# Optimization experiments

Hardware: AMD Instinct MI355X
Metric: run time of the kernel (lower is better)

## Reference

```python
import jax, jax.numpy as jnp
import numpy as np

B, S, DA, DV, DU, L, M = 16, 256, 1, 32, 1, 4, 12


def conv1x1(x, w, b):
    # x: [B,C,H,W], w: [O,C], b: [O]
    return jnp.einsum('bchw,oc->bohw', x, w) + b[None, :, None, None]


def setup_inputs() -> dict:
    key = jax.random.key(0)
    ks = jax.random.split(key, 12)
    sc = 0.02
    return {
        'x':    jax.random.normal(ks[0], (B, S, S, DA), dtype=jnp.float32),
        'p_w':  sc * jax.random.normal(ks[1], (DV, DA + 2), dtype=jnp.float32),
        'p_b':  sc * jax.random.normal(ks[2], (DV,), dtype=jnp.float32),
        'ws_w': sc * jax.random.normal(ks[3], (L, DV, DV), dtype=jnp.float32),
        'ws_b': sc * jax.random.normal(ks[4], (L, DV), dtype=jnp.float32),
        'w1r':  sc * jax.random.normal(ks[5], (L, DV, DV, M, M), dtype=jnp.float32),
        'w1i':  sc * jax.random.normal(ks[6], (L, DV, DV, M, M), dtype=jnp.float32),
        'w2r':  sc * jax.random.normal(ks[7], (L, DV, DV, M, M), dtype=jnp.float32),
        'w2i':  sc * jax.random.normal(ks[8], (L, DV, DV, M, M), dtype=jnp.float32),
        'q_w':  sc * jax.random.normal(ks[9], (DU, DV), dtype=jnp.float32),
        'q_b':  sc * jax.random.normal(ks[10], (DU,), dtype=jnp.float32),
    }


def fourier_layer(x, w1r, w1i, w2r, w2i):
    # x: [B,C,H,W]; FFT norm None == 'backward' (numpy/jax default)
    b, c, h, w = x.shape
    x_ft = jnp.fft.rfft2(x)                       # [B,C,H,W//2+1] complex
    W1 = w1r + 1j * w1i                           # [C,C,M,M]
    W2 = w2r + 1j * w2i
    top = jnp.einsum('bixy,ioxy->boxy', x_ft[:, :, :M, :M], W1)
    bot = jnp.einsum('bixy,ioxy->boxy', x_ft[:, :, -M:, :M], W2)
    out_ft = jnp.zeros((b, c, h, w // 2 + 1), dtype=x_ft.dtype)
    out_ft = out_ft.at[:, :, :M, :M].set(top)
    out_ft = out_ft.at[:, :, h - M:, :M].set(bot)
    return jnp.fft.irfft2(out_ft, s=(h, w))


def reference(x, p_w, p_b, ws_w, ws_b, w1r, w1i, w2r, w2i, q_w, q_b):
    b, sx, sy, _ = x.shape
    # grid as in get_grid (requires sx == sy, as the original implicitly does)
    gx = jnp.linspace(-1.0, 1.0, sx, dtype=jnp.float32)
    gy = jnp.linspace(-1.0, 1.0, sy, dtype=jnp.float32)
    gridx = jnp.broadcast_to(gx.reshape(1, 1, sx, 1), (b, sy, sx, 1))
    gridy = jnp.broadcast_to(gy.reshape(1, sy, 1, 1), (b, sy, sx, 1))
    grid = jnp.concatenate([gridy, gridx], axis=-1)     # [B,Sy,Sx,2]
    h = jnp.concatenate([x, grid], axis=-1)             # [B,S,S,DA+2]
    h = jnp.transpose(h, (0, 3, 1, 2))                  # NCHW
    h = conv1x1(h, p_w, p_b)                            # lifting
    for i in range(L):
        x1 = fourier_layer(h, w1r[i], w1i[i], w2r[i], w2i[i])
        x2 = conv1x1(h, ws_w[i], ws_b[i])
        h = x1 + x2
        if i < L - 1:
            h = jax.nn.relu(h)
    h = conv1x1(h, q_w, q_b)                            # projection -> [B,1,S,S]
    return jnp.transpose(h, (0, 2, 3, 1)).squeeze(-1)   # [B,S,S]
```

## Files before the change

kernel.cpp:

```cpp
#include <hip/hip_runtime.h>
#include <math.h>

#define NB 16
#define SS 256
#define DV 32
#define MM 12
#define MK 24
#define LL 4
#define TWO_PI_N 0.024543692606170259679f
#define TSTR 65


__global__ __launch_bounds__(256) void k_prep(const float* __restrict__ ws_w,
        float* __restrict__ twT, float* __restrict__ wT, float* __restrict__ tw2)
{
    int j = threadIdx.x;
    #pragma unroll
    for (int k = 0; k < MM; ++k) {
        float ang = TWO_PI_N * (float)((k * j) & 255);
        float s, c; sincosf(ang, &s, &c);
        twT[j * (MM * 2) + 2 * k]     = c;
        twT[j * (MM * 2) + 2 * k + 1] = -s;
        tw2[(k * SS + j) * 2]     = c;
        tw2[(k * SS + j) * 2 + 1] = s;
    }
    for (int idx = threadIdx.x; idx < LL * DV * DV; idx += 256) {
        int l = idx >> 10, rem = idx & 1023, co = rem >> 5, ci = rem & 31;
        wT[(l * DV + ci) * DV + co] = ws_w[(l * DV + co) * DV + ci];
    }
}

__global__ __launch_bounds__(256) void k_lift(const float* __restrict__ x,
        const float* __restrict__ p_w, const float* __restrict__ p_b,
        float* __restrict__ h)
{
    int tid = threadIdx.x;
    int lane = tid & 63;
    int w = __builtin_amdgcn_readfirstlane(tid >> 6);
    int b  = blockIdx.x >> 6;
    int iy = ((blockIdx.x & 63) << 2) + w;
    int j0 = lane << 2;

    float4 xv = *(const float4*)(x + ((size_t)(b * SS + iy)) * SS + j0);
    float gy = -1.f + 2.f * (float)iy * (1.f / 255.f);
    float4 gx;
    gx.x = -1.f + 2.f * (float)j0 * (1.f / 255.f);
    gx.y = gx.x + 2.f / 255.f; gx.z = gx.y + 2.f / 255.f; gx.w = gx.z + 2.f / 255.f;

    float* hb = h + ((size_t)b * DV * SS + iy) * SS + j0;
    #pragma unroll
    for (int c = 0; c < DV; ++c) {
        float w0 = p_w[3*c], w1 = p_w[3*c+1], w2 = p_w[3*c+2], bb = p_b[c];
        float4 v;
        v.x = w0 * xv.x + w1 * gy + w2 * gx.x + bb;
        v.y = w0 * xv.y + w1 * gy + w2 * gx.y + bb;
        v.z = w0 * xv.z + w1 * gy + w2 * gx.z + bb;
        v.w = w0 * xv.w + w1 * gy + w2 * gx.w + bb;
        *(float4*)(hb + (size_t)c * SS * SS) = v;
    }
}

__global__ __launch_bounds__(512, 4) void k_rowdft(const float* __restrict__ h,
        const float* __restrict__ twT, float* __restrict__ A)
{
    __shared__ float smem[SS * TSTR];
    int tid = threadIdx.x;
    int iy = tid & 255;
    int half = __builtin_amdgcn_readfirstlane(tid >> 8);
    int b = blockIdx.x >> 5, c = blockIdx.x & 31;
    const float* hrow = h + (size_t)blockIdx.x * SS * SS;

    float ar[MM], ai[MM];
    #pragma unroll
    for (int k = 0; k < MM; ++k) { ar[k] = 0.f; ai[k] = 0.f; }

    for (int t = 0; t < 4; ++t) {
        int jb = t * 64;
        __syncthreads();
        #pragma unroll
        for (int k = 0; k < 8; ++k) {
            int idx = tid + k * 512;
            int row = idx >> 4, col4 = idx & 15;
            float4 v = *(const float4*)(hrow + (size_t)row * SS + jb + col4 * 4);
            float* d = &smem[row * TSTR + col4 * 4];
            d[0] = v.x; d[1] = v.y; d[2] = v.z; d[3] = v.w;
        }
        __syncthreads();
        const float* rp = &smem[iy * TSTR + half * 32];
        #pragma unroll
        for (int jq = 0; jq < 8; ++jq) {
            #pragma unroll
            for (int u = 0; u < 4; ++u) {
                float v = rp[jq * 4 + u];
                const float* twj = twT + (size_t)(jb + half * 32 + jq * 4 + u)
                                         * (MM * 2);
                #pragma unroll
                for (int k = 0; k < 6; ++k) {
                    ar[2*k]   += v * twj[4*k];
                    ai[2*k]   += v * twj[4*k + 1];
                    ar[2*k+1] += v * twj[4*k + 2];
                    ai[2*k+1] += v * twj[4*k + 3];
                }
            }
        }
    }

    __syncthreads();
    if (half == 0) {
        #pragma unroll
        for (int k = 0; k < MM; ++k) {
            smem[(2*k) * SS + iy]     = ar[k];
            smem[(2*k + 1) * SS + iy] = ai[k];
        }
    }
    __syncthreads();
    if (half == 1) {
        #pragma unroll
        for (int ky = 0; ky < MM; ++ky) {
            float2 val;
            val.x = ar[ky] + smem[(2*ky) * SS + iy];
            val.y = ai[ky] + smem[(2*ky + 1) * SS + iy];
            size_t o = ((((size_t)b * MM + ky) * DV + c) * SS + iy) * 2;
            *(float2*)&A[o] = val;
        }
    }
}

__global__ __launch_bounds__(256, 4) void k_cm(const float* __restrict__ A,
        const float* __restrict__ w1r, const float* __restrict__ w1i,
        const float* __restrict__ w2r, const float* __restrict__ w2i,
        float* __restrict__ F, int l)
{
    __shared__ float FinS[DV][6][2];
    int blk = blockIdx.x;
    int mg = blk & 3;
    int bk = blk >> 2;
    int ky = bk % MM;
    int tid = threadIdx.x;
    int c = tid >> 3, ch = tid & 7;
    int iy0 = ch * 32;

    const float2* Ap = (const float2*)(A + ((size_t)bk * DV + c) * SS * 2);

    float fr[6], fi[6], pc[6], ps[6], sc[6], ssn[6];
    #pragma unroll
    for (int k = 0; k < 6; ++k) {
        int m = mg * 6 + k;
        int f = (m < MM) ? m : (232 + m);
        float s, cc;
        sincosf(TWO_PI_N * (float)f, &s, &cc);
        sc[k] = cc; ssn[k] = s;
        sincosf(TWO_PI_N * (float)((f * iy0) & 255), &s, &cc);
        pc[k] = cc; ps[k] = s;
        fr[k] = fi[k] = 0.f;
    }
    #pragma unroll 4
    for (int i = 0; i < 32; ++i) {
        float2 a = Ap[iy0 + i];
        #pragma unroll
        for (int k = 0; k < 6; ++k) {
            fr[k] += a.x * pc[k] + a.y * ps[k];
            fi[k] += a.y * pc[k] - a.x * ps[k];
            float np = pc[k] * sc[k] - ps[k] * ssn[k];
            float nq = pc[k] * ssn[k] + ps[k] * sc[k];
            pc[k] = np; ps[k] = nq;
        }
    }
    #pragma unroll
    for (int m = 1; m < 8; m <<= 1) {
        #pragma unroll
        for (int k = 0; k < 6; ++k) {
            fr[k] += __shfl_xor(fr[k], m, 64);
            fi[k] += __shfl_xor(fi[k], m, 64);
        }
    }
    #pragma unroll
    for (int k = 0; k < 6; ++k) {
        if (ch == k) { FinS[c][k][0] = fr[k]; FinS[c][k][1] = fi[k]; }
    }
    __syncthreads();

    if (ch < 6) {
        int o = c;
        int m = mg * 6 + ch;
        const float* Wr; const float* Wi; int xm;
        if (m < MM) { Wr = w1r; Wi = w1i; xm = m; }
        else        { Wr = w2r; Wi = w2i; xm = m - MM; }
        float scale = ((ky == 0) ? 1.0f : 2.0f) * (1.0f / 65536.0f);
        float orr = 0.f, oii = 0.f;
        #pragma unroll 4
        for (int i = 0; i < DV; ++i) {
            float gr = FinS[i][ch][0], gi = FinS[i][ch][1];
            size_t wi = ((size_t)(l * DV + i) * DV + o) * (MM * MM) + xm * MM + ky;
            float wr = Wr[wi], wim = Wi[wi];
            orr += gr * wr - gi * wim;
            oii += gr * wim + gi * wr;
        }
        size_t off = (((size_t)bk * MK + m) * DV + o) * 2;
        F[off] = orr * scale; F[off + 1] = oii * scale;
    }
}

__global__ __launch_bounds__(384) void k_inv1(const float* __restrict__ F,
        float* __restrict__ g)
{
    __shared__ float itw[MK * 2];
    int tid = threadIdx.x;
    int b = blockIdx.x >> 8, iy = blockIdx.x & 255;
    if (tid < MK) {
        int f = (tid < MM) ? tid : (232 + tid);
        float ang = TWO_PI_N * (float)((f * iy) & 255);
        float s, c; sincosf(ang, &s, &c);
        itw[2 * tid] = c; itw[2 * tid + 1] = s;
    }
    __syncthreads();

    int ky = tid >> 5, co = tid & 31;
    const float* Fp = F + ((size_t)(b * MM + ky) * MK) * (DV * 2) + 2 * co;
    float gr = 0.f, gi = 0.f;
    #pragma unroll
    for (int m = 0; m < MK; ++m) {
        float2 fv = *(const float2*)(Fp + (size_t)m * (DV * 2));
        float ic = itw[2 * m], is = itw[2 * m + 1];
        gr += fv.x * ic - fv.y * is;
        gi += fv.x * is + fv.y * ic;
    }
    size_t o = (((size_t)(b * SS + iy)) * MM + ky) * (DV * 2) + 2 * co;
    g[o] = gr; g[o + 1] = gi;
}

template<int FINAL>
__global__ __launch_bounds__(256, 4) void k_pt(float* __restrict__ h,
        const float* __restrict__ g, const float* __restrict__ wT,
        const float* __restrict__ ws_b, const float* __restrict__ tw2,
        const float* __restrict__ q_w, const float* __restrict__ q_b,
        float* __restrict__ out, int l)
{
    int tid = threadIdx.x;
    int lane = tid & 63;
    int w = __builtin_amdgcn_readfirstlane(tid >> 6);
    int b  = blockIdx.x >> 7;
    int iy = ((blockIdx.x & 127) << 1) + (w >> 1);
    int j0 = ((w & 1) << 7) + (lane << 1);

    float* hb = h + ((size_t)b * DV * SS + iy) * SS + j0;
    const float* wt  = wT + (size_t)l * DV * DV;
    const float* wsb = ws_b + (size_t)l * DV;

    float2 acc[DV];
    #pragma unroll
    for (int co = 0; co < DV; ++co) {
        float bv = wsb[co];
        acc[co].x = bv; acc[co].y = bv;
    }

    #pragma unroll 4
    for (int ci = 0; ci < DV; ++ci) {
        float2 hv = *(const float2*)(hb + (size_t)ci * SS * SS);
        const float* wc = wt + ci * DV;
        #pragma unroll
        for (int co = 0; co < DV; ++co) {
            float wv = wc[co];
            acc[co].x += wv * hv.x; acc[co].y += wv * hv.y;
        }
    }

    const float* gp = g + ((size_t)(b * SS + iy)) * (MM * DV * 2);
    #pragma unroll 2
    for (int ky = 0; ky < MM; ++ky) {
        float4 t4 = *(const float4*)(tw2 + ((size_t)ky * SS + j0) * 2);
        const float* Gk = gp + ky * (DV * 2);
        #pragma unroll
        for (int co = 0; co < DV; ++co) {
            float gr = Gk[2 * co], gi = Gk[2 * co + 1];
            acc[co].x += gr * t4.x - gi * t4.y;
            acc[co].y += gr * t4.z - gi * t4.w;
        }
    }

    if (FINAL) {
        float qb = q_b[0];
        float2 o2; o2.x = qb; o2.y = qb;
        #pragma unroll
        for (int co = 0; co < DV; ++co) {
            float qv = q_w[co];
            o2.x += qv * acc[co].x; o2.y += qv * acc[co].y;
        }
        *(float2*)(out + ((size_t)(b * SS + iy)) * SS + j0) = o2;
    } else {
        #pragma unroll
        for (int co = 0; co < DV; ++co) {
            float2 v;
            v.x = fmaxf(acc[co].x, 0.f); v.y = fmaxf(acc[co].y, 0.f);
            *(float2*)(hb + (size_t)co * SS * SS) = v;
        }
    }
}

extern "C" void kernel_launch(void* const* d_in, const int* in_sizes, int n_in,
                              void* d_out, int out_size, void* d_ws, size_t ws_size,
                              hipStream_t stream)
{
    const float* x    = (const float*)d_in[0];
    const float* p_w  = (const float*)d_in[1];
    const float* p_b  = (const float*)d_in[2];
    const float* ws_w = (const float*)d_in[3];
    const float* ws_b = (const float*)d_in[4];
    const float* w1r  = (const float*)d_in[5];
    const float* w1i  = (const float*)d_in[6];
    const float* w2r  = (const float*)d_in[7];
    const float* w2i  = (const float*)d_in[8];
    const float* q_w  = (const float*)d_in[9];
    const float* q_b  = (const float*)d_in[10];
    float* out = (float*)d_out;

    float* h   = (float*)d_ws;
    float* A   = h   + (size_t)NB * DV * SS * SS;
    float* F   = A   + (size_t)NB * MM * DV * SS * 2;
    float* g   = F   + (size_t)NB * MM * MK * DV * 2;
    float* twT = g   + (size_t)NB * SS * MM * DV * 2;
    float* wT  = twT + (size_t)SS * MM * 2;
    float* tw2 = wT  + (size_t)LL * DV * DV;

    dim3 blk(256);
    k_prep<<<1, blk, 0, stream>>>(ws_w, twT, wT, tw2);
    k_lift<<<NB * 64, blk, 0, stream>>>(x, p_w, p_b, h);
    for (int l = 0; l < LL; ++l) {
        k_rowdft<<<NB * DV, dim3(512), 0, stream>>>(h, twT, A);
        k_cm<<<NB * MM * 4, blk, 0, stream>>>(A, w1r, w1i, w2r, w2i, F, l);
        k_inv1<<<NB * SS, dim3(384), 0, stream>>>(F, g);
        if (l < LL - 1)
            k_pt<0><<<NB * 128, blk, 0, stream>>>(h, g, wT, ws_b, tw2,
                                                  nullptr, nullptr, nullptr, l);
        else
            k_pt<1><<<NB * 128, blk, 0, stream>>>(h, g, wT, ws_b, tw2,
                                                  q_w, q_b, out, l);
    }
}
```

Baseline: 708.3 us.

## Fuse row DFT into lift and pointwise kernels via LDS staging

Removes the standalone row-DFT kernel. The lift and pointwise-update kernels now also stage their freshly computed h rows (2 rows × 32 channels) in LDS and compute the truncated row DFT from there, writing A directly. This avoids re-reading the full h tensor from global memory for each layer and drops one launch per layer. In exchange the fused kernels need more LDS and run at lower occupancy (launch bounds 2). The per-thread DFT loop also covers 64 samples serially, followed by an LDS reduction across 4 wave partials.

```diff
diff --git a/kernel.cpp b/kernel.cpp
--- a/kernel.cpp
+++ b/kernel.cpp
@@ -8,7 +8,7 @@
 #define MK 24
 #define LL 4
 #define TWO_PI_N 0.024543692606170259679f
-#define TSTR 65
+#define TSTR2 258
 
 
 __global__ __launch_bounds__(256) void k_prep(const float* __restrict__ ws_w,
@@ -30,100 +30,87 @@
     }
 }
 
-__global__ __launch_bounds__(256) void k_lift(const float* __restrict__ x,
+__device__ __forceinline__ void row_dft_lds(float* smem,
+        const float* __restrict__ twT, float* __restrict__ A,
+        int b, int iyp, int tid)
+{
+    int lane = tid & 63;
+    int jq = __builtin_amdgcn_readfirstlane(tid >> 6);
+    int row = lane >> 5, c = lane & 31;
+
+    const float* rp = &smem[(row * DV + c) * TSTR2 + jq * 64];
+    float ar[MM], ai[MM];
+    #pragma unroll
+    for (int k = 0; k < MM; ++k) { ar[k] = 0.f; ai[k] = 0.f; }
+
+    #pragma unroll 4
+    for (int i = 0; i < 64; ++i) {
+        float v = rp[i];
+        const float* twj = twT + (size_t)(jq * 64 + i) * (MM * 2);
+        #pragma unroll
+        for (int k = 0; k < 6; ++k) {
+            ar[2*k]   += v * twj[4*k];
+            ai[2*k]   += v * twj[4*k + 1];
+            ar[2*k+1] += v * twj[4*k + 2];
+            ai[2*k+1] += v * twj[4*k + 3];
+        }
+    }
+
+    __syncthreads();
+    float* pp = &smem[(size_t)((jq * 2 + row) * DV + c) * 25];
+    #pragma unroll
+    for (int k = 0; k < MM; ++k) { pp[2*k] = ar[k]; pp[2*k + 1] = ai[k]; }
+    __syncthreads();
+
+    int row2 = tid >> 7, c2 = (tid >> 2) & 31, kg = tid & 3;
+    int iy = iyp * 2 + row2;
+    #pragma unroll
+    for (int kk = 0; kk < 3; ++kk) {
+        int ky = kg * 3 + kk;
+        float sr = 0.f, si = 0.f;
+        #pragma unroll
+        for (int q = 0; q < 4; ++q) {
+            const float* qq = &smem[(size_t)((q * 2 + row2) * DV + c2) * 25 + 2 * ky];
+            sr += qq[0]; si += qq[1];
+        }
+        size_t o = ((((size_t)b * MM + ky) * DV + c2) * SS + iy) * 2;
+        float2 val; val.x = sr; val.y = si;
+        *(float2*)&A[o] = val;
+    }
+}
+
+__global__ __launch_bounds__(256, 2) void k_liftA(const float* __restrict__ x,
         const float* __restrict__ p_w, const float* __restrict__ p_b,
-        float* __restrict__ h)
-{
+        float* __restrict__ h, const float* __restrict__ twT,
+        float* __restrict__ A)
+{
+    __shared__ float smem[2 * DV * TSTR2];
     int tid = threadIdx.x;
     int lane = tid & 63;
     int w = __builtin_amdgcn_readfirstlane(tid >> 6);
-    int b  = blockIdx.x >> 6;
-    int iy = ((blockIdx.x & 63) << 2) + w;
-    int j0 = lane << 2;
-
-    float4 xv = *(const float4*)(x + ((size_t)(b * SS + iy)) * SS + j0);
-    float gy = -1.f + 2.f * (float)iy * (1.f / 255.f);
-    float4 gx;
-    gx.x = -1.f + 2.f * (float)j0 * (1.f / 255.f);
-    gx.y = gx.x + 2.f / 255.f; gx.z = gx.y + 2.f / 255.f; gx.w = gx.z + 2.f / 255.f;
+    int b   = blockIdx.x >> 7;
+    int iyp = blockIdx.x & 127;
+    int row = w >> 1;
+    int iy  = iyp * 2 + row;
+    int j0  = ((w & 1) << 7) + (lane << 1);
+
+    float2 xv = *(const float2*)(x + ((size_t)(b * SS + iy)) * SS + j0);
+    float gy  = -1.f + 2.f * (float)iy * (1.f / 255.f);
+    float gxa = -1.f + 2.f * (float)j0 * (1.f / 255.f);
+    float gxb = gxa + 2.f / 255.f;
 
     float* hb = h + ((size_t)b * DV * SS + iy) * SS + j0;
     #pragma unroll
     for (int c = 0; c < DV; ++c) {
         float w0 = p_w[3*c], w1 = p_w[3*c+1], w2 = p_w[3*c+2], bb = p_b[c];
-        float4 v;
-        v.x = w0 * xv.x + w1 * gy + w2 * gx.x + bb;
-        v.y = w0 * xv.y + w1 * gy + w2 * gx.y + bb;
-        v.z = w0 * xv.z + w1 * gy + w2 * gx.z + bb;
-        v.w = w0 * xv.w + w1 * gy + w2 * gx.w + bb;
-        *(float4*)(hb + (size_t)c * SS * SS) = v;
-    }
-}
-
-__global__ __launch_bounds__(512, 4) void k_rowdft(const float* __restrict__ h,
-        const float* __restrict__ twT, float* __restrict__ A)
-{
-    __shared__ float smem[SS * TSTR];
-    int tid = threadIdx.x;
-    int iy = tid & 255;
-    int half = __builtin_amdgcn_readfirstlane(tid >> 8);
-    int b = blockIdx.x >> 5, c = blockIdx.x & 31;
-    const float* hrow = h + (size_t)blockIdx.x * SS * SS;
-
-    float ar[MM], ai[MM];
-    #pragma unroll
-    for (int k = 0; k < MM; ++k) { ar[k] = 0.f; ai[k] = 0.f; }
-
-    for (int t = 0; t < 4; ++t) {
-        int jb = t * 64;
-        __syncthreads();
-        #pragma unroll
-        for (int k = 0; k < 8; ++k) {
-            int idx = tid + k * 512;
-            int row = idx >> 4, col4 = idx & 15;
-            float4 v = *(const float4*)(hrow + (size_t)row * SS + jb + col4 * 4);
-            float* d = &smem[row * TSTR + col4 * 4];
-            d[0] = v.x; d[1] = v.y; d[2] = v.z; d[3] = v.w;
-        }
-        __syncthreads();
-        const float* rp = &smem[iy * TSTR + half * 32];
-        #pragma unroll
-        for (int jq = 0; jq < 8; ++jq) {
-            #pragma unroll
-            for (int u = 0; u < 4; ++u) {
-                float v = rp[jq * 4 + u];
-                const float* twj = twT + (size_t)(jb + half * 32 + jq * 4 + u)
-                                         * (MM * 2);
-                #pragma unroll
-                for (int k = 0; k < 6; ++k) {
-                    ar[2*k]   += v * twj[4*k];
-                    ai[2*k]   += v * twj[4*k + 1];
-                    ar[2*k+1] += v * twj[4*k + 2];
-                    ai[2*k+1] += v * twj[4*k + 3];
-                }
-            }
-        }
-    }
-
-    __syncthreads();
-    if (half == 0) {
-        #pragma unroll
-        for (int k = 0; k < MM; ++k) {
-            smem[(2*k) * SS + iy]     = ar[k];
-            smem[(2*k + 1) * SS + iy] = ai[k];
-        }
-    }
-    __syncthreads();
-    if (half == 1) {
-        #pragma unroll
-        for (int ky = 0; ky < MM; ++ky) {
-            float2 val;
-            val.x = ar[ky] + smem[(2*ky) * SS + iy];
-            val.y = ai[ky] + smem[(2*ky + 1) * SS + iy];
-            size_t o = ((((size_t)b * MM + ky) * DV + c) * SS + iy) * 2;
-            *(float2*)&A[o] = val;
-        }
-    }
+        float2 v;
+        v.x = w0 * xv.x + w1 * gy + w2 * gxa + bb;
+        v.y = w0 * xv.y + w1 * gy + w2 * gxb + bb;
+        *(float2*)(hb + (size_t)c * SS * SS) = v;
+        *(float2*)&smem[(size_t)(row * DV + c) * TSTR2 + j0] = v;
+    }
+    __syncthreads();
+    row_dft_lds(smem, twT, A, b, iyp, tid);
 }
 
 __global__ __launch_bounds__(256, 4) void k_cm(const float* __restrict__ A,
@@ -229,8 +216,68 @@
     g[o] = gr; g[o + 1] = gi;
 }
 
-template<int FINAL>
-__global__ __launch_bounds__(256, 4) void k_pt(float* __restrict__ h,
+__global__ __launch_bounds__(256, 2) void k_ptA(float* __restrict__ h,
+        const float* __restrict__ g, const float* __restrict__ wT,
+        const float* __restrict__ ws_b, const float* __restrict__ tw2,
+        const float* __restrict__ twT, float* __restrict__ A, int l)
+{
+    __shared__ float smem[2 * DV * TSTR2];
+    int tid = threadIdx.x;
+    int lane = tid & 63;
+    int w = __builtin_amdgcn_readfirstlane(tid >> 6);
+    int b   = blockIdx.x >> 7;
+    int iyp = blockIdx.x & 127;
+    int row = w >> 1;
+    int iy  = iyp * 2 + row;
+    int j0  = ((w & 1) << 7) + (lane << 1);
+
+    float* hb = h + ((size_t)b * DV * SS + iy) * SS + j0;
+    const float* wt  = wT + (size_t)l * DV * DV;
+    const float* wsb = ws_b + (size_t)l * DV;
+
+    float2 acc[DV];
+    #pragma unroll
+    for (int co = 0; co < DV; ++co) {
+        float bv = wsb[co];
+        acc[co].x = bv; acc[co].y = bv;
+    }
+
+    #pragma unroll 4
+    for (int ci = 0; ci < DV; ++ci) {
+        float2 hv = *(const float2*)(hb + (size_t)ci * SS * SS);
+        const float* wc = wt + ci * DV;
+        #pragma unroll
+        for (int co = 0; co < DV; ++co) {
+            float wv = wc[co];
+            acc[co].x += wv * hv.x; acc[co].y += wv * hv.y;
+        }
+    }
+
+    const float* gp = g + ((size_t)(b * SS + iy)) * (MM * DV * 2);
+    #pragma unroll 2
+    for (int ky = 0; ky < MM; ++ky) {
+        float4 t4 = *(const float4*)(tw2 + ((size_t)ky * SS + j0) * 2);
+        const float* Gk = gp + ky * (DV * 2);
+        #pragma unroll
+        for (int co = 0; co < DV; ++co) {
+            float gr = Gk[2 * co], gi = Gk[2 * co + 1];
+            acc[co].x += gr * t4.x - gi * t4.y;
+            acc[co].y += gr * t4.z - gi * t4.w;
+        }
+    }
+
+    #pragma unroll
+    for (int co = 0; co < DV; ++co) {
+        float2 v;
+        v.x = fmaxf(acc[co].x, 0.f); v.y = fmaxf(acc[co].y, 0.f);
+        *(float2*)(hb + (size_t)co * SS * SS) = v;
+        *(float2*)&smem[(size_t)(row * DV + co) * TSTR2 + j0] = v;
+    }
+    __syncthreads();
+    row_dft_lds(smem, twT, A, b, iyp, tid);
+}
+
+__global__ __launch_bounds__(256, 4) void k_final(const float* __restrict__ h,
         const float* __restrict__ g, const float* __restrict__ wT,
         const float* __restrict__ ws_b, const float* __restrict__ tw2,
         const float* __restrict__ q_w, const float* __restrict__ q_b,
@@ -243,7 +290,7 @@
     int iy = ((blockIdx.x & 127) << 1) + (w >> 1);
     int j0 = ((w & 1) << 7) + (lane << 1);
 
-    float* hb = h + ((size_t)b * DV * SS + iy) * SS + j0;
+    const float* hb = h + ((size_t)b * DV * SS + iy) * SS + j0;
     const float* wt  = wT + (size_t)l * DV * DV;
     const float* wsb = ws_b + (size_t)l * DV;
 
@@ -278,23 +325,14 @@
         }
     }
 
-    if (FINAL) {
-        float qb = q_b[0];
-        float2 o2; o2.x = qb; o2.y = qb;
-        #pragma unroll
-        for (int co = 0; co < DV; ++co) {
-            float qv = q_w[co];
-            o2.x += qv * acc[co].x; o2.y += qv * acc[co].y;
-        }
-        *(float2*)(out + ((size_t)(b * SS + iy)) * SS + j0) = o2;
-    } else {
-        #pragma unroll
-        for (int co = 0; co < DV; ++co) {
-            float2 v;
-            v.x = fmaxf(acc[co].x, 0.f); v.y = fmaxf(acc[co].y, 0.f);
-            *(float2*)(hb + (size_t)co * SS * SS) = v;
-        }
-    }
+    float qb = q_b[0];
+    float2 o2; o2.x = qb; o2.y = qb;
+    #pragma unroll
+    for (int co = 0; co < DV; ++co) {
+        float qv = q_w[co];
+        o2.x += qv * acc[co].x; o2.y += qv * acc[co].y;
+    }
+    *(float2*)(out + ((size_t)(b * SS + iy)) * SS + j0) = o2;
 }
 
 extern "C" void kernel_launch(void* const* d_in, const int* in_sizes, int n_in,
@@ -324,16 +362,14 @@
 
     dim3 blk(256);
     k_prep<<<1, blk, 0, stream>>>(ws_w, twT, wT, tw2);
-    k_lift<<<NB * 64, blk, 0, stream>>>(x, p_w, p_b, h);
+    k_liftA<<<NB * 128, blk, 0, stream>>>(x, p_w, p_b, h, twT, A);
     for (int l = 0; l < LL; ++l) {
-        k_rowdft<<<NB * DV, dim3(512), 0, stream>>>(h, twT, A);
         k_cm<<<NB * MM * 4, blk, 0, stream>>>(A, w1r, w1i, w2r, w2i, F, l);
         k_inv1<<<NB * SS, dim3(384), 0, stream>>>(F, g);
         if (l < LL - 1)
-            k_pt<0><<<NB * 128, blk, 0, stream>>>(h, g, wT, ws_b, tw2,
-                                                  nullptr, nullptr, nullptr, l);
+            k_ptA<<<NB * 128, blk, 0, stream>>>(h, g, wT, ws_b, tw2, twT, A, l);
         else
-            k_pt<1><<<NB * 128, blk, 0, stream>>>(h, g, wT, ws_b, tw2,
+            k_final<<<NB * 128, blk, 0, stream>>>(h, g, wT, ws_b, tw2,
                                                   q_w, q_b, out, l);
     }
 }
```

Result: slower. 787.0 us (+11.1%).

## Split row DFT across two half-row blocks with 4-way column partition

Applied to the files above, without the earlier changes.

The row-DFT kernel now launches two blocks per (batch, channel) plane, each handling 128 rows. The 512 threads split the columns four ways in 32-column tiles, using a smaller shared buffer, and combine partial sums with a two-step shared-memory tree reduction. This doubles the grid and shrinks LDS use so more blocks fit per CU, at the cost of extra reduction syncs. Launch-bound occupancy hints are also raised for k_rowdft and k_pt.

```diff
diff --git a/kernel.cpp b/kernel.cpp
--- a/kernel.cpp
+++ b/kernel.cpp
@@ -8,7 +8,7 @@
 #define MK 24
 #define LL 4
 #define TWO_PI_N 0.024543692606170259679f
-#define TSTR 65
+#define TSTR 33
 
 
 __global__ __launch_bounds__(256) void k_prep(const float* __restrict__ ws_w,
@@ -60,67 +60,84 @@
     }
 }
 
-__global__ __launch_bounds__(512, 4) void k_rowdft(const float* __restrict__ h,
+__global__ __launch_bounds__(512, 8) void k_rowdft(const float* __restrict__ h,
         const float* __restrict__ twT, float* __restrict__ A)
 {
-    __shared__ float smem[SS * TSTR];
-    int tid = threadIdx.x;
-    int iy = tid & 255;
-    int half = __builtin_amdgcn_readfirstlane(tid >> 8);
-    int b = blockIdx.x >> 5, c = blockIdx.x & 31;
-    const float* hrow = h + (size_t)blockIdx.x * SS * SS;
+    __shared__ float smem[6336];
+    int tid = threadIdx.x;
+    int iy = tid & 127;
+    int jq = __builtin_amdgcn_readfirstlane(tid >> 7);
+    int bc = blockIdx.x >> 1;
+    int iyh = blockIdx.x & 1;
+    int b = bc >> 5, c = bc & 31;
+    const float* hrow = h + (size_t)bc * SS * SS + (size_t)iyh * 128 * SS;
 
     float ar[MM], ai[MM];
     #pragma unroll
     for (int k = 0; k < MM; ++k) { ar[k] = 0.f; ai[k] = 0.f; }
 
-    for (int t = 0; t < 4; ++t) {
-        int jb = t * 64;
+    for (int t = 0; t < 8; ++t) {
+        int jb = t * 32;
         __syncthreads();
         #pragma unroll
-        for (int k = 0; k < 8; ++k) {
+        for (int k = 0; k < 2; ++k) {
             int idx = tid + k * 512;
-            int row = idx >> 4, col4 = idx & 15;
+            int row = idx >> 3, col4 = idx & 7;
             float4 v = *(const float4*)(hrow + (size_t)row * SS + jb + col4 * 4);
             float* d = &smem[row * TSTR + col4 * 4];
             d[0] = v.x; d[1] = v.y; d[2] = v.z; d[3] = v.w;
         }
         __syncthreads();
-        const float* rp = &smem[iy * TSTR + half * 32];
-        #pragma unroll
-        for (int jq = 0; jq < 8; ++jq) {
+        const float* rp = &smem[iy * TSTR + jq * 8];
+        #pragma unroll
+        for (int i = 0; i < 8; ++i) {
+            float v = rp[i];
+            const float* twj = twT + (size_t)(jb + jq * 8 + i) * (MM * 2);
             #pragma unroll
-            for (int u = 0; u < 4; ++u) {
-                float v = rp[jq * 4 + u];
-                const float* twj = twT + (size_t)(jb + half * 32 + jq * 4 + u)
-                                         * (MM * 2);
-                #pragma unroll
-                for (int k = 0; k < 6; ++k) {
-                    ar[2*k]   += v * twj[4*k];
-                    ai[2*k]   += v * twj[4*k + 1];
-                    ar[2*k+1] += v * twj[4*k + 2];
-                    ai[2*k+1] += v * twj[4*k + 3];
-                }
+            for (int k = 0; k < 6; ++k) {
+                ar[2*k]   += v * twj[4*k];
+                ai[2*k]   += v * twj[4*k + 1];
+                ar[2*k+1] += v * twj[4*k + 2];
+                ai[2*k+1] += v * twj[4*k + 3];
             }
         }
     }
 
     __syncthreads();
-    if (half == 0) {
+    if (jq & 1) {
+        float* rd = &smem[(jq >> 1) * 3072];
         #pragma unroll
         for (int k = 0; k < MM; ++k) {
-            smem[(2*k) * SS + iy]     = ar[k];
-            smem[(2*k + 1) * SS + iy] = ai[k];
-        }
-    }
-    __syncthreads();
-    if (half == 1) {
+            rd[(2*k) * 128 + iy]     = ar[k];
+            rd[(2*k + 1) * 128 + iy] = ai[k];
+        }
+    }
+    __syncthreads();
+    if (!(jq & 1)) {
+        const float* rd = &smem[(jq >> 1) * 3072];
+        #pragma unroll
+        for (int k = 0; k < MM; ++k) {
+            ar[k] += rd[(2*k) * 128 + iy];
+            ai[k] += rd[(2*k + 1) * 128 + iy];
+        }
+    }
+    __syncthreads();
+    if (jq == 2) {
+        #pragma unroll
+        for (int k = 0; k < MM; ++k) {
+            smem[(2*k) * 128 + iy]     = ar[k];
+            smem[(2*k + 1) * 128 + iy] = ai[k];
+        }
+    }
+    __syncthreads();
+    if (jq == 0) {
+        int iyg = iyh * 128 + iy;
         #pragma unroll
         for (int ky = 0; ky < MM; ++ky) {
             float2 val;
-            val.x = ar[ky] + smem[(2*ky) * SS + iy];
-            val.y = ai[ky] + smem[(2*ky + 1) * SS + iy];
-            size_t o = ((((size_t)b * MM + ky) * DV + c) * SS + iy) * 2;
+            val.x = ar[ky] + smem[(2*ky) * 128 + iy];
+            val.y = ai[ky] + smem[(2*ky + 1) * 128 + iy];
+            size_t o = ((((size_t)b * MM + ky) * DV + c) * SS + iyg) * 2;
             *(float2*)&A[o] = val;
         }
     }
@@ -230,7 +247,7 @@
 }
 
 template<int FINAL>
-__global__ __launch_bounds__(256, 4) void k_pt(float* __restrict__ h,
+__global__ __launch_bounds__(256, 8) void k_pt(float* __restrict__ h,
         const float* __restrict__ g, const float* __restrict__ wT,
         const float* __restrict__ ws_b, const float* __restrict__ tw2,
         const float* __restrict__ q_w, const float* __restrict__ q_b,
@@ -326,7 +343,7 @@
     k_prep<<<1, blk, 0, stream>>>(ws_w, twT, wT, tw2);
     k_lift<<<NB * 64, blk, 0, stream>>>(x, p_w, p_b, h);
     for (int l = 0; l < LL; ++l) {
-        k_rowdft<<<NB * DV, dim3(512), 0, stream>>>(h, twT, A);
+        k_rowdft<<<NB * DV * 2, dim3(512), 0, stream>>>(h, twT, A);
         k_cm<<<NB * MM * 4, blk, 0, stream>>>(A, w1r, w1i, w2r, w2i, F, l);
         k_inv1<<<NB * SS, dim3(384), 0, stream>>>(F, g);
         if (l < LL - 1)
```

Result: slower. 2.398 ms (+238.6%).
